# Kernel optimization log

Hardware: AMD Instinct MI355X
Metric: run time of the kernel (lower is better)

Reference implementation:

```python
import jax, jax.numpy as jnp
import numpy as np

EPS = 1e-8  # RMSNormMultiHead default eps (forward passes self.eps)


def rms_norm_multihead(x, weight):
    # x: (B, L, H, d); normalize over last dim in float32, then scale per (H, d)
    x32 = x.astype(jnp.float32)
    normed = x32 * jax.lax.rsqrt(jnp.mean(x32 * x32, axis=-1, keepdims=True) + EPS)
    return normed.astype(x.dtype) * weight


def setup_inputs() -> dict:
    key = jax.random.key(0)
    k0, k1, k2 = jax.random.split(key, 3)
    B, L, D, H = 2, 1024, 1024, 16
    d = D // H
    X = jax.random.normal(k0, (B, L, D), dtype=jnp.float32)
    Wq = jax.random.normal(k1, (D, D), dtype=jnp.float32) * 0.02  # q_proj weight (out, in)
    Wv = jax.random.normal(k2, (D, D), dtype=jnp.float32) * 0.02  # v_proj weight (out, in)
    q_norm_w = jnp.ones((H, d), dtype=jnp.float32)
    v_norm_w = jnp.ones((H, d), dtype=jnp.float32)
    return {"X": X, "Wq": Wq, "Wv": Wv, "q_norm_w": q_norm_w, "v_norm_w": v_norm_w}


def reference(X, Wq, Wv, q_norm_w, v_norm_w):
    B, L, D = X.shape
    H, d = q_norm_w.shape
    K = X.reshape(B, L, H, d)
    Q = rms_norm_multihead((X @ Wq.T).reshape(B, L, H, d), q_norm_w)
    V = rms_norm_multihead((X @ Wv.T).reshape(B, L, H, d), v_norm_w)
    # cumulative outer-product KV state: (B, L, H, d, e)
    W = jnp.cumsum(jnp.einsum('blhd,blhe->blhde', K, V), axis=1)
    out = jnp.einsum('blhd,blhde->blhe', Q, W).reshape(B, L, D)
    return out
```

## Files before the change

kernel.cpp:

```cpp
#include <hip/hip_runtime.h>

#define BB 2
#define LL 1024
#define DD 1024
#define HH 16
#define NC 16
#define EPSF 1e-8f

typedef __attribute__((ext_vector_type(8))) short bf16x8;
typedef __attribute__((ext_vector_type(4))) float f32x4;
typedef unsigned short u16;

static __device__ inline u16 f2bf(float f) {
    unsigned int u = __builtin_bit_cast(unsigned int, f);
    u += 0x7fff + ((u >> 16) & 1);
    return (u16)(u >> 16);
}
static __device__ inline float bf2f(u16 v) {
    unsigned int u = ((unsigned int)v) << 16;
    return __builtin_bit_cast(float, u);
}
static __device__ inline void gload_lds16(const u16* g, u16* l) {
    __builtin_amdgcn_global_load_lds((const __attribute__((address_space(1))) void*)g,
                                     (__attribute__((address_space(3))) void*)l, 16, 0, 0);
}

__global__ __launch_bounds__(256) void cvt_k(const float* __restrict__ X,
                                             const float* __restrict__ Wq,
                                             const float* __restrict__ Wv,
                                             u16* __restrict__ Xb,
                                             u16* __restrict__ Wqb,
                                             u16* __restrict__ Wvb)
{
    int i = (blockIdx.x * 256 + threadIdx.x) * 4;
    const float* s; u16* d; int off;
    if (i < 2*1024*1024)      { s = X;  d = Xb;  off = i; }
    else if (i < 3*1024*1024) { s = Wq; d = Wqb; off = i - 2*1024*1024; }
    else                      { s = Wv; d = Wvb; off = i - 3*1024*1024; }
    float4 v = *(const float4*)(s + off);
    ushort4 o;
    o.x = f2bf(v.x); o.y = f2bf(v.y); o.z = f2bf(v.z); o.w = f2bf(v.w);
    *(ushort4*)(d + off) = o;
}

__global__ __launch_bounds__(256) void gemm_fused(const u16* __restrict__ Xb,
                                                  const u16* __restrict__ Wqb,
                                                  const u16* __restrict__ Wvb,
                                                  const float* __restrict__ qw,
                                                  const float* __restrict__ vw,
                                                  u16* __restrict__ Qb,
                                                  u16* __restrict__ Vb)
{
    const int K = DD, N = DD;
    const u16* W = blockIdx.z ? Wvb : Wqb;
    const float* nw = blockIdx.z ? vw : qw;
    u16* Y = blockIdx.z ? Vb : Qb;
    __shared__ u16 As0[128 * 32], As1[128 * 32];
    __shared__ u16 Bs0[64 * 32],  Bs1[64 * 32];

    const int tid = threadIdx.x, w = tid >> 6, lane = tid & 63;
    const int quad = lane >> 4, l16 = lane & 15;
    const int m0 = blockIdx.y * 128, n0 = blockIdx.x * 64;
    const int lrow = lane >> 2, lcol = (lane & 3) * 8;

    const u16* gA0 = Xb + (size_t)(m0 + w*16 + lrow) * K + lcol;
    const u16* gA1 = gA0 + (size_t)64 * K;
    const u16* gB0 = W + (size_t)(n0 + w*16 + lrow) * K + lcol;
    u16* lA0_0 = &As0[(w*16) * 32];      u16* lA0_1 = &As1[(w*16) * 32];
    u16* lA1_0 = &As0[(64 + w*16) * 32]; u16* lA1_1 = &As1[(64 + w*16) * 32];
    u16* lB0_0 = &Bs0[(w*16) * 32];      u16* lB0_1 = &Bs1[(w*16) * 32];

    f32x4 acc[2][4] = {};
    for (int k0 = 0; k0 < K; k0 += 64) {
        gload_lds16(gA0 + k0,      lA0_0);
        gload_lds16(gA0 + k0 + 32, lA0_1);
        gload_lds16(gA1 + k0,      lA1_0);
        gload_lds16(gA1 + k0 + 32, lA1_1);
        gload_lds16(gB0 + k0,      lB0_0);
        gload_lds16(gB0 + k0 + 32, lB0_1);
        __syncthreads();
        #pragma unroll
        for (int hh = 0; hh < 2; ++hh) {
            const u16* Ah = hh ? As1 : As0;
            const u16* Bh = hh ? Bs1 : Bs0;
            bf16x8 af[2], bfr[4];
            #pragma unroll
            for (int i = 0; i < 2; ++i)
                af[i] = *(const bf16x8*)&Ah[(w*32 + i*16 + l16) * 32 + quad*8];
            #pragma unroll
            for (int j = 0; j < 4; ++j)
                bfr[j] = *(const bf16x8*)&Bh[(j*16 + l16) * 32 + quad*8];
            #pragma unroll
            for (int i = 0; i < 2; ++i)
                #pragma unroll
                for (int j = 0; j < 4; ++j)
                    acc[i][j] = __builtin_amdgcn_mfma_f32_16x16x32_bf16(af[i], bfr[j], acc[i][j], 0, 0, 0);
        }
        __syncthreads();
    }

    float wv4[4];
    #pragma unroll
    for (int j = 0; j < 4; ++j) wv4[j] = nw[n0 + j*16 + l16];
    #pragma unroll
    for (int i = 0; i < 2; ++i) {
        float ss[4];
        #pragma unroll
        for (int r = 0; r < 4; ++r) {
            float s = 0.f;
            #pragma unroll
            for (int j = 0; j < 4; ++j) s += acc[i][j][r] * acc[i][j][r];
            ss[r] = s;
        }
        #pragma unroll
        for (int off = 1; off < 16; off <<= 1)
            #pragma unroll
            for (int r = 0; r < 4; ++r) ss[r] += __shfl_xor(ss[r], off, 64);
        float sc[4];
        #pragma unroll
        for (int r = 0; r < 4; ++r) sc[r] = rsqrtf(ss[r] * (1.f/64.f) + EPSF);
        #pragma unroll
        for (int r = 0; r < 4; ++r) {
            u16* yp = Y + (size_t)(m0 + w*32 + i*16 + quad*4 + r) * N + n0;
            #pragma unroll
            for (int j = 0; j < 4; ++j)
                yp[j*16 + l16] = f2bf(acc[i][j][r] * sc[r] * wv4[j]);
        }
    }
}

__global__ __launch_bounds__(256) void kv_chunk(const u16* __restrict__ Xb,
                                                const u16* __restrict__ Vb,
                                                u16* __restrict__ S)
{
    const int c = blockIdx.x & 15, bh = blockIdx.x >> 4;
    const int h = bh & 15, b = bh >> 4;
    __shared__ u16 Kt[64][72];
    __shared__ u16 Vt[64][72];
    const int tid = threadIdx.x;
    {
        const int row = tid >> 2, q = tid & 3;
        size_t gbase = (size_t)(b*LL + c*64 + row) * DD + h*64 + q*16;
        u16 kk[16], vv[16];
        #pragma unroll
        for (int i = 0; i < 16; i += 4) {
            *(ushort4*)&kk[i] = *(const ushort4*)(Xb + gbase + i);
            *(ushort4*)&vv[i] = *(const ushort4*)(Vb + gbase + i);
        }
        #pragma unroll
        for (int i = 0; i < 16; ++i) {
            Kt[q*16 + i][row] = kk[i];
            Vt[q*16 + i][row] = vv[i];
        }
    }
    __syncthreads();
    const int w = tid >> 6, lane = tid & 63, quad = lane >> 4, l16 = lane & 15;
    const int me = (w & 1) * 32, nd = (w >> 1) * 32;
    f32x4 acc[2][2] = {};
    #pragma unroll
    for (int k0 = 0; k0 < 64; k0 += 32) {
        bf16x8 av[2], bv[2];
        #pragma unroll
        for (int i = 0; i < 2; ++i)
            av[i] = *(const bf16x8*)&Vt[me + i*16 + l16][k0 + quad*8];
        #pragma unroll
        for (int j = 0; j < 2; ++j)
            bv[j] = *(const bf16x8*)&Kt[nd + j*16 + l16][k0 + quad*8];
        #pragma unroll
        for (int i = 0; i < 2; ++i)
            #pragma unroll
            for (int j = 0; j < 2; ++j)
                acc[i][j] = __builtin_amdgcn_mfma_f32_16x16x32_bf16(av[i], bv[j], acc[i][j], 0, 0, 0);
    }
    u16* Sp = S + ((size_t)blockIdx.x << 12) + w*1024;
    #pragma unroll
    for (int i = 0; i < 2; ++i)
        #pragma unroll
        for (int j = 0; j < 2; ++j)
            #pragma unroll
            for (int r = 0; r < 4; ++r)
                Sp[(i*2 + j)*256 + r*64 + lane] = f2bf(acc[i][j][r]);
}

__global__ __launch_bounds__(256) void out_k2(const u16* __restrict__ Xb,
                                              const u16* __restrict__ Qb,
                                              const u16* __restrict__ Vb,
                                              const u16* __restrict__ S,
                                              float* __restrict__ out)
{
    const int c = 15 - (blockIdx.x & 15);
    const int bh = blockIdx.x >> 4;
    const int h = bh & 15, b = bh >> 4;
    __shared__ u16 Qs[64][72];
    __shared__ u16 Ks[64][72];
    __shared__ u16 Vt[64][72];
    __shared__ u16 St[64][72];
    const int tid = threadIdx.x;
    {
        const int row = tid >> 2, q = tid & 3;
        size_t gbase = (size_t)(b*LL + c*64 + row) * DD + h*64 + q*16;
        u16 vv[16];
        #pragma unroll
        for (int i = 0; i < 16; i += 4) {
            *(ushort4*)&Qs[row][q*16 + i] = *(const ushort4*)(Qb + gbase + i);
            *(ushort4*)&Ks[row][q*16 + i] = *(const ushort4*)(Xb + gbase + i);
            *(ushort4*)&vv[i] = *(const ushort4*)(Vb + gbase + i);
        }
        #pragma unroll
        for (int i = 0; i < 16; ++i)
            Vt[q*16 + i][row] = vv[i];
        float facc[16] = {};
        const u16* Sbase = S + ((size_t)(bh * NC) << 12);
        for (int cp = 0; cp < c; ++cp) {
            const u16* Sc = Sbase + ((size_t)cp << 12);
            #pragma unroll
            for (int jj = 0; jj < 4; ++jj) {
                ushort4 sv = *(const ushort4*)(Sc + tid*4 + jj*1024);
                facc[jj*4+0] += bf2f(sv.x);
                facc[jj*4+1] += bf2f(sv.y);
                facc[jj*4+2] += bf2f(sv.z);
                facc[jj*4+3] += bf2f(sv.w);
            }
        }
        #pragma unroll
        for (int jj = 0; jj < 4; ++jj) {
            int g = tid * 4;
            int ij = (g >> 8) & 3, r = (g >> 6) & 3, ln = g & 63;
            int e = (jj & 1)*32 + (ij >> 1)*16 + (ln >> 4)*4 + r;
            int d = (jj >> 1)*32 + (ij & 1)*16 + (ln & 15);
            ushort4 o;
            o.x = f2bf(facc[jj*4+0]);
            o.y = f2bf(facc[jj*4+1]);
            o.z = f2bf(facc[jj*4+2]);
            o.w = f2bf(facc[jj*4+3]);
            *(ushort4*)&St[e][d] = o;
        }
    }
    __syncthreads();
    const int w = tid >> 6, lane = tid & 63, quad = lane >> 4, l16 = lane & 15;
    const int mo = (w & 1) * 32, no = (w >> 1) * 32;

    f32x4 pacc[2][2] = {};
    #pragma unroll
    for (int k0 = 0; k0 < 64; k0 += 32) {
        bf16x8 aq[2], bk[2];
        #pragma unroll
        for (int i = 0; i < 2; ++i)
            aq[i] = *(const bf16x8*)&Qs[mo + i*16 + l16][k0 + quad*8];
        #pragma unroll
        for (int j = 0; j < 2; ++j)
            bk[j] = *(const bf16x8*)&Ks[no + j*16 + l16][k0 + quad*8];
        #pragma unroll
        for (int i = 0; i < 2; ++i)
            #pragma unroll
            for (int j = 0; j < 2; ++j)
                pacc[i][j] = __builtin_amdgcn_mfma_f32_16x16x32_bf16(aq[i], bk[j], pacc[i][j], 0, 0, 0);
    }
    __syncthreads();
    #pragma unroll
    for (int i = 0; i < 2; ++i)
        #pragma unroll
        for (int j = 0; j < 2; ++j)
            #pragma unroll
            for (int r = 0; r < 4; ++r) {
                int l  = mo + i*16 + quad*4 + r;
                int lp = no + j*16 + l16;
                Ks[l][lp] = (lp <= l) ? f2bf(pacc[i][j][r]) : (u16)0;
            }
    __syncthreads();

    f32x4 acc[2][2] = {};
    #pragma unroll
    for (int k0 = 0; k0 < 64; k0 += 32) {
        bf16x8 a1[2], b1[2], a2[2], b2[2];
        #pragma unroll
        for (int i = 0; i < 2; ++i) {
            a1[i] = *(const bf16x8*)&Ks[mo + i*16 + l16][k0 + quad*8];
            a2[i] = *(const bf16x8*)&Qs[mo + i*16 + l16][k0 + quad*8];
        }
        #pragma unroll
        for (int j = 0; j < 2; ++j) {
            b1[j] = *(const bf16x8*)&Vt[no + j*16 + l16][k0 + quad*8];
            b2[j] = *(const bf16x8*)&St[no + j*16 + l16][k0 + quad*8];
        }
        #pragma unroll
        for (int i = 0; i < 2; ++i)
            #pragma unroll
            for (int j = 0; j < 2; ++j) {
                acc[i][j] = __builtin_amdgcn_mfma_f32_16x16x32_bf16(a1[i], b1[j], acc[i][j], 0, 0, 0);
                acc[i][j] = __builtin_amdgcn_mfma_f32_16x16x32_bf16(a2[i], b2[j], acc[i][j], 0, 0, 0);
            }
    }
    float* op = out + (size_t)(b*LL + c*64) * DD + h*64;
    #pragma unroll
    for (int i = 0; i < 2; ++i)
        #pragma unroll
        for (int j = 0; j < 2; ++j)
            #pragma unroll
            for (int r = 0; r < 4; ++r)
                op[(size_t)(mo + i*16 + quad*4 + r) * DD + no + j*16 + l16] = acc[i][j][r];
}

extern "C" void kernel_launch(void* const* d_in, const int* in_sizes, int n_in,
                              void* d_out, int out_size, void* d_ws, size_t ws_size,
                              hipStream_t stream) {
    const float* X  = (const float*)d_in[0];
    const float* Wq = (const float*)d_in[1];
    const float* Wv = (const float*)d_in[2];
    const float* qw = (const float*)d_in[3];
    const float* vw = (const float*)d_in[4];
    float* out = (float*)d_out;

    u16* Xb  = (u16*)d_ws;
    u16* Wqb = Xb  + (size_t)2*1024*1024;
    u16* Wvb = Wqb + (size_t)1024*1024;
    u16* Qb  = Wvb + (size_t)1024*1024;
    u16* Vb  = Qb  + (size_t)2*1024*1024;
    u16* S   = Vb  + (size_t)2*1024*1024;

    cvt_k<<<4096, 256, 0, stream>>>(X, Wq, Wv, Xb, Wqb, Wvb);
    gemm_fused<<<dim3(16, 16, 2), 256, 0, stream>>>(Xb, Wqb, Wvb, qw, vw, Qb, Vb);
    kv_chunk<<<BB*HH*NC, 256, 0, stream>>>(Xb, Vb, S);
    out_k2<<<BB*HH*NC, 256, 0, stream>>>(Xb, Qb, Vb, S, out);
}
```

Before: 104.1 us.

## Fuse per-chunk KV outer products into the V-projection GEMM epilogue and swizzle LDS

Removes the separate kv_chunk kernel. V-projection blocks now stage their normalized V tile and the matching X (K) tile in LDS and compute the two per-chunk K^T V partial states directly, saving a launch and a reload of Xb/Vb from global memory. It also XOR-swizzles the LDS layout of the GEMM A/B tiles to reduce bank conflicts, and unrolls the S prefix-sum loop in out_k2 by two. The extra 34 KB of LDS per block may lower GEMM occupancy, and only the z=1 blocks take on the added epilogue work, so the load across blocks becomes uneven.

```diff
diff --git a/kernel.cpp b/kernel.cpp
--- a/kernel.cpp
+++ b/kernel.cpp
@@ -49,7 +49,8 @@
                                                   const float* __restrict__ qw,
                                                   const float* __restrict__ vw,
                                                   u16* __restrict__ Qb,
-                                                  u16* __restrict__ Vb)
+                                                  u16* __restrict__ Vb,
+                                                  u16* __restrict__ S)
 {
     const int K = DD, N = DD;
     const u16* W = blockIdx.z ? Wvb : Wqb;
@@ -57,11 +58,14 @@
     u16* Y = blockIdx.z ? Vb : Qb;
     __shared__ u16 As0[128 * 32], As1[128 * 32];
     __shared__ u16 Bs0[64 * 32],  Bs1[64 * 32];
+    __shared__ u16 Vt[64][136];
+    __shared__ u16 Kt[64][136];
 
     const int tid = threadIdx.x, w = tid >> 6, lane = tid & 63;
     const int quad = lane >> 4, l16 = lane & 15;
     const int m0 = blockIdx.y * 128, n0 = blockIdx.x * 64;
-    const int lrow = lane >> 2, lcol = (lane & 3) * 8;
+    const int lrow = lane >> 2;
+    const int lcol = ((lane & 3) ^ ((lane >> 3) & 3)) * 8;
 
     const u16* gA0 = Xb + (size_t)(m0 + w*16 + lrow) * K + lcol;
     const u16* gA1 = gA0 + (size_t)64 * K;
@@ -69,6 +73,8 @@
     u16* lA0_0 = &As0[(w*16) * 32];      u16* lA0_1 = &As1[(w*16) * 32];
     u16* lA1_0 = &As0[(64 + w*16) * 32]; u16* lA1_1 = &As1[(64 + w*16) * 32];
     u16* lB0_0 = &Bs0[(w*16) * 32];      u16* lB0_1 = &Bs1[(w*16) * 32];
+
+    const int sw = (quad ^ ((l16 >> 1) & 3)) * 8;
 
     f32x4 acc[2][4] = {};
     for (int k0 = 0; k0 < K; k0 += 64) {
@@ -86,10 +92,10 @@
             bf16x8 af[2], bfr[4];
             #pragma unroll
             for (int i = 0; i < 2; ++i)
-                af[i] = *(const bf16x8*)&Ah[(w*32 + i*16 + l16) * 32 + quad*8];
+                af[i] = *(const bf16x8*)&Ah[(w*32 + i*16 + l16) * 32 + sw];
             #pragma unroll
             for (int j = 0; j < 4; ++j)
-                bfr[j] = *(const bf16x8*)&Bh[(j*16 + l16) * 32 + quad*8];
+                bfr[j] = *(const bf16x8*)&Bh[(j*16 + l16) * 32 + sw];
             #pragma unroll
             for (int i = 0; i < 2; ++i)
                 #pragma unroll
@@ -123,63 +129,59 @@
         for (int r = 0; r < 4; ++r) {
             u16* yp = Y + (size_t)(m0 + w*32 + i*16 + quad*4 + r) * N + n0;
             #pragma unroll
-            for (int j = 0; j < 4; ++j)
-                yp[j*16 + l16] = f2bf(acc[i][j][r] * sc[r] * wv4[j]);
-        }
-    }
-}
-
-__global__ __launch_bounds__(256) void kv_chunk(const u16* __restrict__ Xb,
-                                                const u16* __restrict__ Vb,
-                                                u16* __restrict__ S)
-{
-    const int c = blockIdx.x & 15, bh = blockIdx.x >> 4;
-    const int h = bh & 15, b = bh >> 4;
-    __shared__ u16 Kt[64][72];
-    __shared__ u16 Vt[64][72];
-    const int tid = threadIdx.x;
-    {
-        const int row = tid >> 2, q = tid & 3;
-        size_t gbase = (size_t)(b*LL + c*64 + row) * DD + h*64 + q*16;
-        u16 kk[16], vv[16];
-        #pragma unroll
-        for (int i = 0; i < 16; i += 4) {
-            *(ushort4*)&kk[i] = *(const ushort4*)(Xb + gbase + i);
-            *(ushort4*)&vv[i] = *(const ushort4*)(Vb + gbase + i);
-        }
-        #pragma unroll
-        for (int i = 0; i < 16; ++i) {
-            Kt[q*16 + i][row] = kk[i];
-            Vt[q*16 + i][row] = vv[i];
-        }
-    }
-    __syncthreads();
-    const int w = tid >> 6, lane = tid & 63, quad = lane >> 4, l16 = lane & 15;
-    const int me = (w & 1) * 32, nd = (w >> 1) * 32;
-    f32x4 acc[2][2] = {};
-    #pragma unroll
-    for (int k0 = 0; k0 < 64; k0 += 32) {
-        bf16x8 av[2], bv[2];
-        #pragma unroll
-        for (int i = 0; i < 2; ++i)
-            av[i] = *(const bf16x8*)&Vt[me + i*16 + l16][k0 + quad*8];
-        #pragma unroll
-        for (int j = 0; j < 2; ++j)
-            bv[j] = *(const bf16x8*)&Kt[nd + j*16 + l16][k0 + quad*8];
-        #pragma unroll
-        for (int i = 0; i < 2; ++i)
-            #pragma unroll
-            for (int j = 0; j < 2; ++j)
-                acc[i][j] = __builtin_amdgcn_mfma_f32_16x16x32_bf16(av[i], bv[j], acc[i][j], 0, 0, 0);
-    }
-    u16* Sp = S + ((size_t)blockIdx.x << 12) + w*1024;
-    #pragma unroll
-    for (int i = 0; i < 2; ++i)
-        #pragma unroll
-        for (int j = 0; j < 2; ++j)
-            #pragma unroll
-            for (int r = 0; r < 4; ++r)
-                Sp[(i*2 + j)*256 + r*64 + lane] = f2bf(acc[i][j][r]);
+            for (int j = 0; j < 4; ++j) {
+                u16 val = f2bf(acc[i][j][r] * sc[r] * wv4[j]);
+                yp[j*16 + l16] = val;
+                if (blockIdx.z)
+                    Vt[j*16 + l16][w*32 + i*16 + quad*4 + r] = val;
+            }
+        }
+    }
+
+    if (blockIdx.z) {
+        {
+            const int row = tid >> 1, q2 = tid & 1;
+            size_t gb = (size_t)(m0 + row) * DD + n0 + q2 * 32;
+            u16 kk[32];
+            #pragma unroll
+            for (int i2 = 0; i2 < 32; i2 += 4)
+                *(ushort4*)&kk[i2] = *(const ushort4*)(Xb + gb + i2);
+            #pragma unroll
+            for (int i2 = 0; i2 < 32; ++i2)
+                Kt[q2*32 + i2][row] = kk[i2];
+        }
+        __syncthreads();
+        const int me = (w & 1) * 32, nd = (w >> 1) * 32;
+        const int b = m0 >> 10, c0 = (m0 & 1023) >> 6, h = blockIdx.x;
+        const int bh = b * HH + h;
+        #pragma unroll
+        for (int cc = 0; cc < 2; ++cc) {
+            f32x4 sacc[2][2] = {};
+            #pragma unroll
+            for (int k0 = 0; k0 < 64; k0 += 32) {
+                bf16x8 av[2], bv[2];
+                #pragma unroll
+                for (int i2 = 0; i2 < 2; ++i2)
+                    av[i2] = *(const bf16x8*)&Vt[me + i2*16 + l16][cc*64 + k0 + quad*8];
+                #pragma unroll
+                for (int j2 = 0; j2 < 2; ++j2)
+                    bv[j2] = *(const bf16x8*)&Kt[nd + j2*16 + l16][cc*64 + k0 + quad*8];
+                #pragma unroll
+                for (int i2 = 0; i2 < 2; ++i2)
+                    #pragma unroll
+                    for (int j2 = 0; j2 < 2; ++j2)
+                        sacc[i2][j2] = __builtin_amdgcn_mfma_f32_16x16x32_bf16(av[i2], bv[j2], sacc[i2][j2], 0, 0, 0);
+            }
+            u16* Sp = S + ((size_t)((bh << 4) | (c0 + cc)) << 12) + w*1024;
+            #pragma unroll
+            for (int i2 = 0; i2 < 2; ++i2)
+                #pragma unroll
+                for (int j2 = 0; j2 < 2; ++j2)
+                    #pragma unroll
+                    for (int r = 0; r < 4; ++r)
+                        Sp[(i2*2 + j2)*256 + r*64 + lane] = f2bf(sacc[i2][j2][r]);
+        }
+    }
 }
 
 __global__ __launch_bounds__(256) void out_k2(const u16* __restrict__ Xb,
@@ -211,7 +213,21 @@
             Vt[q*16 + i][row] = vv[i];
         float facc[16] = {};
         const u16* Sbase = S + ((size_t)(bh * NC) << 12);
-        for (int cp = 0; cp < c; ++cp) {
+        int cp = 0;
+        for (; cp + 2 <= c; cp += 2) {
+            const u16* Sc0 = Sbase + ((size_t)cp << 12);
+            const u16* Sc1 = Sc0 + 4096;
+            #pragma unroll
+            for (int jj = 0; jj < 4; ++jj) {
+                ushort4 sv0 = *(const ushort4*)(Sc0 + tid*4 + jj*1024);
+                ushort4 sv1 = *(const ushort4*)(Sc1 + tid*4 + jj*1024);
+                facc[jj*4+0] += bf2f(sv0.x); facc[jj*4+0] += bf2f(sv1.x);
+                facc[jj*4+1] += bf2f(sv0.y); facc[jj*4+1] += bf2f(sv1.y);
+                facc[jj*4+2] += bf2f(sv0.z); facc[jj*4+2] += bf2f(sv1.z);
+                facc[jj*4+3] += bf2f(sv0.w); facc[jj*4+3] += bf2f(sv1.w);
+            }
+        }
+        if (cp < c) {
             const u16* Sc = Sbase + ((size_t)cp << 12);
             #pragma unroll
             for (int jj = 0; jj < 4; ++jj) {
@@ -319,7 +335,6 @@
     u16* S   = Vb  + (size_t)2*1024*1024;
 
     cvt_k<<<4096, 256, 0, stream>>>(X, Wq, Wv, Xb, Wqb, Wvb);
-    gemm_fused<<<dim3(16, 16, 2), 256, 0, stream>>>(Xb, Wqb, Wvb, qw, vw, Qb, Vb);
-    kv_chunk<<<BB*HH*NC, 256, 0, stream>>>(Xb, Vb, S);
+    gemm_fused<<<dim3(16, 16, 2), 256, 0, stream>>>(Xb, Wqb, Wvb, qw, vw, Qb, Vb, S);
     out_k2<<<BB*HH*NC, 256, 0, stream>>>(Xb, Qb, Vb, S, out);
 }
```

After: 99.01 us. 1.05x faster.
